# Kernel tuning notes

Measured on AMD Instinct MI355X. Metric: run time of the kernel, lower is better.

## Reference

```python
import jax, jax.numpy as jnp
import numpy as np

B, S, D = 8, 2048, 64
H = 128


def setup_inputs() -> dict:
    key = jax.random.key(0)
    k = jax.random.split(key, 5)
    X = jax.random.normal(k[0], (B, S, D), dtype=jnp.float32)
    Wi = jax.random.normal(k[1], (H, D), dtype=jnp.float32)          # init_layer weight, std=1
    bi = jax.random.normal(k[2], (H,), dtype=jnp.float32)            # init_layer bias, std=1
    Wa = jax.random.normal(k[3], (H * H, D + 1), dtype=jnp.float32) / jnp.sqrt(H)  # vf_A, std=1/sqrt(H)
    Wb = jax.random.normal(k[4], (H, D + 1), dtype=jnp.float32)      # vf_B, std=1
    return {"X": X, "Wi": Wi, "bi": bi, "Wa": Wa, "Wb": Wb}


def reference(X, Wi, bi, Wa, Wb):
    b, s, d = X.shape
    dt = 1.0 / (s - 1)
    # inp: time channel (constant dt) concatenated with scaled input -> [b, s, d+1]
    inp = jnp.concatenate([jnp.full((b, s, 1), dt, dtype=X.dtype), X * dt], axis=-1)
    y0 = X[:, 0] @ Wi.T + bi                       # [b, H]
    Bs = jnp.einsum('bsk,hk->bsh', inp[:, 1:], Wb)  # [b, s-1, H]

    def step(y, xs):
        inp_t, b_t = xs                            # [b, d+1], [b, H]
        A = (inp_t @ Wa.T).reshape(b, H, H)        # per-step transition matrix
        y_new = y + jnp.einsum('bij,bj->bi', A, y) + b_t
        return y_new, y_new

    xs = (jnp.swapaxes(inp[:, 1:], 0, 1), jnp.swapaxes(Bs, 0, 1))  # time-major
    _, ys_rest = jax.lax.scan(step, y0, xs)        # [s-1, b, H]
    ys = jnp.concatenate([y0[:, None, :], jnp.swapaxes(ys_rest, 0, 1)], axis=1)
    return ys
```

## Files before the change

### kernel.cpp

```cpp
#include <hip/hip_runtime.h>
#include <hip/hip_fp16.h>


typedef _Float16 h8 __attribute__((ext_vector_type(8)));
typedef float v4f __attribute__((ext_vector_type(4)));
typedef unsigned int uint;

constexpr int B_ = 8, S_ = 2048, D_ = 64, H_ = 128;
constexpr int T_ = S_ - 1;
constexpr int KD = D_ + 1;
constexpr float DTC = 1.0f / 2047.0f;
constexpr int L_ = 8;
constexpr int LSH = 3;
constexpr int NC = 256;

__global__ __launch_bounds__(256) void k_prep0(const float* __restrict__ Wa,
                                               _Float16* __restrict__ Wa16B,
                                               float* __restrict__ Wa0,
                                               const float* __restrict__ X,
                                               _Float16* __restrict__ Xs16) {
  int bx = blockIdx.x;
  if (bx < 4096) {
    int idx = bx * 256 + threadIdx.x;
    int r = idx >> 6, kk = idx & 63;
    int rt = r >> 4, n = r & 15;
    int kb = kk >> 5, q = (kk >> 3) & 3, jj = kk & 7;
    float v = Wa[(size_t)r * KD + 1 + kk];
    Wa16B[((((size_t)rt * 2 + kb) * 4 + q) * 16 + n) * 8 + jj] = (_Float16)v;
    if (kk == 0) Wa0[r] = Wa[(size_t)r * KD];
  } else {
    int idx = (bx - 4096) * 256 + threadIdx.x;
    if (idx < B_ * T_ * 64) {
      int bt = idx >> 6, d = idx & 63;
      int b = bt / T_, s = bt - b * T_;
      Xs16[(size_t)bt * 64 + d] = (_Float16)(X[((size_t)b * S_ + s + 1) * D_ + d] * DTC);
    }
  }
}

__global__ __launch_bounds__(256) void k_prep1(const float* __restrict__ X,
                                               const float* __restrict__ Wb,
                                               float* __restrict__ Bs,
                                               const float* __restrict__ Wi,
                                               const float* __restrict__ bi,
                                               float* __restrict__ out,
                                               float* __restrict__ yb) {
  int tid = threadIdx.x;
  if (blockIdx.x >= 1024) {
    int b = blockIdx.x - 1024;
    __shared__ float xs0[D_];
    if (tid < D_) xs0[tid] = X[(size_t)b * S_ * D_ + tid];
    __syncthreads();
    if (tid < H_) {
      float acc = bi[tid];
      const float* wr = Wi + tid * D_;
#pragma unroll 8
      for (int d = 0; d < D_; d++) acc += xs0[d] * wr[d];
      out[(size_t)b * S_ * H_ + tid] = acc;
      yb[(size_t)(b * NC + 0) * H_ + tid] = acc;
    }
    return;
  }
  __shared__ float wb_s[H_ * KD];
  __shared__ float xs[16][D_ + 4];
  int bt0 = blockIdx.x * 16;
  for (int i = tid; i < H_ * KD; i += 256) wb_s[i] = Wb[i];
  for (int i = tid; i < 16 * D_; i += 256) {
    int sl = i >> 6, d = i & 63;
    int btg = bt0 + sl;
    float v = 0.f;
    if (btg < B_ * T_) {
      int b = btg / T_, s = btg - b * T_;
      v = X[((size_t)b * S_ + s + 1) * D_ + d] * DTC;
    }
    xs[sl][d] = v;
  }
  __syncthreads();
  int h = tid & 127, sh = tid >> 7;
  const float* wrow = &wb_s[h * KD];
  for (int u = 0; u < 8; u++) {
    int sl = sh * 8 + u;
    int btg = bt0 + sl;
    if (btg >= B_ * T_) break;
    float acc = wrow[0] * DTC;
#pragma unroll 8
    for (int d = 0; d < D_; d++) acc += xs[sl][d] * wrow[1 + d];
    Bs[(size_t)btg * H_ + h] = acc;
  }
}

__global__ __launch_bounds__(256) void k_amat(const _Float16* __restrict__ Xs16,
                                              const _Float16* __restrict__ Wa16B,
                                              const float* __restrict__ Wa0,
                                              _Float16* __restrict__ A_sl,
                                              int c0, int scShift) {
  __shared__ _Float16 sb[32 * 528];
  int tid = threadIdx.x;
  int w = tid >> 6, lane = tid & 63;
  int n = lane & 15, q = lane >> 4;
  int rowbase = blockIdx.x * 32;
  int SCm = ((1 << scShift) << LSH) - 1;

  h8 af[2][2];
#pragma unroll
  for (int mi = 0; mi < 2; mi++) {
    int sidx = rowbase + mi * 16 + n;
    int b = sidx >> (scShift + LSH);
    int rem = sidx & SCm;
    int cc = rem >> LSH, l = rem & (L_ - 1);
    int s = (c0 + cc) * L_ + l;
    if (s >= T_) s = T_ - 1;
    size_t btg = (size_t)b * T_ + s;
#pragma unroll
    for (int kb = 0; kb < 2; kb++)
      af[mi][kb] = *(const h8*)(Xs16 + btg * 64 + kb * 32 + q * 8);
  }

  v4f acc[2][8];
#pragma unroll
  for (int nj = 0; nj < 8; nj++) {
    int ct_g = blockIdx.y * 32 + w * 8 + nj;
    float binit = DTC * Wa0[ct_g * 16 + n];
    h8 bf0 = *(const h8*)(Wa16B + ((((size_t)ct_g * 2 + 0) * 4 + q) * 16 + n) * 8);
    h8 bf1 = *(const h8*)(Wa16B + ((((size_t)ct_g * 2 + 1) * 4 + q) * 16 + n) * 8);
#pragma unroll
    for (int mi = 0; mi < 2; mi++) {
      v4f a;
      a[0] = binit; a[1] = binit; a[2] = binit; a[3] = binit;
      a = __builtin_amdgcn_mfma_f32_16x16x32_f16(af[mi][0], bf0, a, 0, 0, 0);
      a = __builtin_amdgcn_mfma_f32_16x16x32_f16(af[mi][1], bf1, a, 0, 0, 0);
      acc[mi][nj] = a;
    }
  }
#pragma unroll
  for (int mi = 0; mi < 2; mi++)
#pragma unroll
    for (int nj = 0; nj < 8; nj++)
#pragma unroll
      for (int reg = 0; reg < 4; reg++)
        sb[(mi * 16 + q * 4 + reg) * 528 + w * 128 + ((nj * 16 + n) ^ (q * 16))] =
            (_Float16)acc[mi][nj][reg];
  __syncthreads();
#pragma unroll
  for (int it = 0; it < 8; it++) {
    int idx = tid + it * 256;
    int t = idx >> 6, u4 = idx & 63;
    int qt = (t >> 2) & 3;
    uint4 val = *(const uint4*)&sb[t * 528 + ((u4 * 8) ^ (qt * 16))];
    *(uint4*)(A_sl + (size_t)(rowbase + t) * 16384 + blockIdx.y * 512 + u4 * 8) = val;
  }
}

__global__ __launch_bounds__(256) void k_chunkmap(const _Float16* __restrict__ A_sl,
                                                  const float* __restrict__ Bs,
                                                  _Float16* __restrict__ Mr,
                                                  float* __restrict__ vch,
                                                  int c0, int scShift) {
  __shared__ _Float16 Dt[128 * 136];
  __shared__ float v32[128];
  int tid = threadIdx.x;
  int w = tid >> 6, lane = tid & 63;
  int n = lane & 15, q = lane >> 4;
  int chunk = blockIdx.x;
  int SC = 1 << scShift;
  int b = chunk >> scShift;
  int cc = chunk & (SC - 1);
  int c = c0 + cc;
  int sbase = c * L_;
  int nsteps = min(L_, T_ - sbase);
  const _Float16* Abase = A_sl + (size_t)chunk * L_ * 16384;
  size_t btb = (size_t)b * T_ + sbase;

#pragma unroll
  for (int it = 0; it < 8; it++) {
    int idx = tid + it * 256;
    int rowl = idx & 127, c8 = (idx >> 7) * 8;
    uint4 pk = *(const uint4*)(Abase + rowl * 128 + c8);
    const _Float16* hp = (const _Float16*)&pk;
#pragma unroll
    for (int cx = 0; cx < 8; cx++) Dt[(c8 + cx) * 136 + rowl] = hp[cx];
  }
  if (tid < 128) v32[tid] = Bs[btb * 128 + tid];
  h8 idE, idO;
#pragma unroll
  for (int jj = 0; jj < 8; jj++) {
    idE[jj] = (_Float16)((q * 8 + jj == n) ? 1.f : 0.f);
    idO[jj] = (_Float16)((q * 8 + jj == 16 + n) ? 1.f : 0.f);
  }
  __syncthreads();

  v4f acc[2][8];
#pragma unroll
  for (int mi = 0; mi < 2; mi++) {
    int row0 = (2 * w + mi) * 16 + q * 4;
#pragma unroll
    for (int nj = 0; nj < 8; nj++) {
      int col = nj * 16 + n;
      union { uint2 u; _Float16 h[4]; } m2;
      m2.u = *(const uint2*)&Dt[col * 136 + row0];
#pragma unroll
      for (int reg = 0; reg < 4; reg++) acc[mi][nj][reg] = (float)m2.h[reg];
    }
  }

  int r0 = 2 * w * 16 + n, r1 = r0 + 16;
  h8 afA[2][4], afB[2][4];

#define LOADA(dst, l)                                                                \
  {                                                                                  \
    const _Float16* Ag = Abase + (size_t)(l) * 16384;                                \
    _Pragma("unroll")                                                                \
    for (int mi = 0; mi < 2; mi++)                                                   \
      _Pragma("unroll")                                                              \
      for (int kb = 0; kb < 4; kb++)                                                 \
        dst[mi][kb] = *(const h8*)(Ag + ((2 * w + mi) * 16 + n) * 128 + kb * 32 + q * 8); \
  }

#define STEPQ(af, l)                                                                 \
  {                                                                                  \
    _Pragma("unroll")                                                                \
    for (int nj = 0; nj < 8; nj++) {                                                 \
      h8 bfr[4];                                                                     \
      _Pragma("unroll")                                                              \
      for (int kb = 0; kb < 4; kb++)                                                 \
        bfr[kb] = *(const h8*)&Dt[(nj * 16 + n) * 136 + kb * 32 + q * 8];            \
      _Pragma("unroll")                                                              \
      for (int mi = 0; mi < 2; mi++) {                                               \
        _Pragma("unroll")                                                            \
        for (int kb = 0; kb < 4; kb++)                                               \
          acc[mi][nj] = __builtin_amdgcn_mfma_f32_16x16x32_f16(af[mi][kb], bfr[kb], acc[mi][nj], 0, 0, 0); \
        acc[mi][nj] = __builtin_amdgcn_mfma_f32_16x16x32_f16(                        \
            af[mi][nj >> 1], (nj & 1) ? idO : idE, acc[mi][nj], 0, 0, 0);            \
      }                                                                              \
    }                                                                                \
    float dv0 = 0.f, dv1 = 0.f;                                                      \
    _Pragma("unroll")                                                                \
    for (int kb = 0; kb < 4; kb++) {                                                 \
      float4 p0 = *(const float4*)&v32[kb * 32 + q * 8];                             \
      float4 p1 = *(const float4*)&v32[kb * 32 + q * 8 + 4];                         \
      float vk[8] = {p0.x, p0.y, p0.z, p0.w, p1.x, p1.y, p1.z, p1.w};                \
      _Pragma("unroll")                                                              \
      for (int jj = 0; jj < 8; jj++) {                                               \
        dv0 += (float)af[0][kb][jj] * vk[jj];                                        \
        dv1 += (float)af[1][kb][jj] * vk[jj];                                        \
      }                                                                              \
    }                                                                                \
    dv0 += __shfl_xor(dv0, 16); dv0 += __shfl_xor(dv0, 32);                          \
    dv1 += __shfl_xor(dv1, 16); dv1 += __shfl_xor(dv1, 32);                          \
    float vold0 = v32[r0], vold1 = v32[r1];                                          \
    float bs0 = 0.f, bs1 = 0.f;                                                      \
    if (q == 0) {                                                                    \
      bs0 = Bs[(btb + (l)) * 128 + r0];                                              \
      bs1 = Bs[(btb + (l)) * 128 + r1];                                              \
    }                                                                                \
    __syncthreads();                                                                 \
    _Pragma("unroll")                                                                \
    for (int mi = 0; mi < 2; mi++) {                                                 \
      int row0 = (2 * w + mi) * 16 + q * 4;                                          \
      _Pragma("unroll")                                                              \
      for (int nj = 0; nj < 8; nj++) {                                               \
        int col = nj * 16 + n;                                                       \
        union { _Float16 h[4]; uint2 u; } pk;                                        \
        _Pragma("unroll")                                                            \
        for (int reg = 0; reg < 4; reg++) pk.h[reg] = (_Float16)acc[mi][nj][reg];    \
        *(uint2*)&Dt[col * 136 + row0] = pk.u;                                       \
      }                                                                              \
    }                                                                                \
    if (q == 0) {                                                                    \
      v32[r0] = vold0 + dv0 + bs0;                                                   \
      v32[r1] = vold1 + dv1 + bs1;                                                   \
    }                                                                                \
    __syncthreads();                                                                 \
  }

  LOADA(afA, 1);
  for (int l = 1; l < nsteps; l += 2) {
    if (l + 1 < nsteps) LOADA(afB, l + 1);
    STEPQ(afA, l);
    if (l + 2 < nsteps) LOADA(afA, l + 2);
    if (l + 1 < nsteps) STEPQ(afB, l + 1);
  }
#undef LOADA
#undef STEPQ

#pragma unroll
  for (int mi = 0; mi < 2; mi++) {
    int row0 = (2 * w + mi) * 16 + q * 4;
#pragma unroll
    for (int nj = 0; nj < 8; nj++) {
      int col = nj * 16 + n;
#pragma unroll
      for (int reg = 0; reg < 4; reg++)
        Dt[(row0 + reg) * 136 + col] = (_Float16)acc[mi][nj][reg];
    }
  }
  __syncthreads();
  _Float16* og = Mr + (size_t)chunk * 16384;
#pragma unroll
  for (int it = 0; it < 8; it++) {
    int idx = tid + it * 256;
    int rowl = idx >> 4, ch = idx & 15;
    uint4 val = *(const uint4*)&Dt[rowl * 136 + ch * 8];
    *(uint4*)(og + rowl * 128 + ch * 8) = val;
  }
  if (tid < 128) vch[(size_t)chunk * 128 + tid] = v32[tid];
}

__global__ __launch_bounds__(256) void k_comp4(const _Float16* __restrict__ in_map,
                                               const float* __restrict__ in_v,
                                               _Float16* __restrict__ out_map,
                                               float* __restrict__ out_v) {
  __shared__ _Float16 Dt[128 * 136];
  __shared__ float v32[128];
  int tid = threadIdx.x;
  int w = tid >> 6, lane = tid & 63;
  int n = lane & 15, q = lane >> 4;
  size_t nbase = (size_t)blockIdx.x * 4;

  const _Float16* P0 = in_map + nbase * 16384;
#pragma unroll
  for (int it = 0; it < 8; it++) {
    int idx = tid + it * 256;
    int rowl = idx & 127, c8 = (idx >> 7) * 8;
    uint4 pk = *(const uint4*)(P0 + rowl * 128 + c8);
    const _Float16* hp = (const _Float16*)&pk;
#pragma unroll
    for (int cx = 0; cx < 8; cx++) Dt[(c8 + cx) * 136 + rowl] = hp[cx];
  }
  if (tid < 128) v32[tid] = in_v[nbase * 128 + tid];
  h8 idE, idO;
#pragma unroll
  for (int jj = 0; jj < 8; jj++) {
    idE[jj] = (_Float16)((q * 8 + jj == n) ? 1.f : 0.f);
    idO[jj] = (_Float16)((q * 8 + jj == 16 + n) ? 1.f : 0.f);
  }
  __syncthreads();

  v4f acc[2][8];
#pragma unroll
  for (int mi = 0; mi < 2; mi++) {
    int row0 = (2 * w + mi) * 16 + q * 4;
#pragma unroll
    for (int nj = 0; nj < 8; nj++) {
      int col = nj * 16 + n;
      union { uint2 u; _Float16 h[4]; } m2;
      m2.u = *(const uint2*)&Dt[col * 136 + row0];
#pragma unroll
      for (int reg = 0; reg < 4; reg++) acc[mi][nj][reg] = (float)m2.h[reg];
    }
  }

  int r0 = 2 * w * 16 + n, r1 = r0 + 16;
  for (int j = 1; j < 4; j++) {
    const _Float16* Pj = in_map + (nbase + j) * 16384;
    h8 af[2][4];
#pragma unroll
    for (int mi = 0; mi < 2; mi++)
#pragma unroll
      for (int kb = 0; kb < 4; kb++)
        af[mi][kb] = *(const h8*)(Pj + ((2 * w + mi) * 16 + n) * 128 + kb * 32 + q * 8);
#pragma unroll
    for (int nj = 0; nj < 8; nj++) {
      h8 bfr[4];
#pragma unroll
      for (int kb = 0; kb < 4; kb++)
        bfr[kb] = *(const h8*)&Dt[(nj * 16 + n) * 136 + kb * 32 + q * 8];
#pragma unroll
      for (int mi = 0; mi < 2; mi++) {
#pragma unroll
        for (int kb = 0; kb < 4; kb++)
          acc[mi][nj] = __builtin_amdgcn_mfma_f32_16x16x32_f16(af[mi][kb], bfr[kb], acc[mi][nj], 0, 0, 0);
        acc[mi][nj] = __builtin_amdgcn_mfma_f32_16x16x32_f16(
            af[mi][nj >> 1], (nj & 1) ? idO : idE, acc[mi][nj], 0, 0, 0);
      }
    }
    float dv0 = 0.f, dv1 = 0.f;
#pragma unroll
    for (int kb = 0; kb < 4; kb++) {
      float4 p0 = *(const float4*)&v32[kb * 32 + q * 8];
      float4 p1 = *(const float4*)&v32[kb * 32 + q * 8 + 4];
      float vk[8] = {p0.x, p0.y, p0.z, p0.w, p1.x, p1.y, p1.z, p1.w};
#pragma unroll
      for (int jj = 0; jj < 8; jj++) {
        dv0 += (float)af[0][kb][jj] * vk[jj];
        dv1 += (float)af[1][kb][jj] * vk[jj];
      }
    }
    dv0 += __shfl_xor(dv0, 16); dv0 += __shfl_xor(dv0, 32);
    dv1 += __shfl_xor(dv1, 16); dv1 += __shfl_xor(dv1, 32);
    float vold0 = v32[r0], vold1 = v32[r1];
    float vj0 = 0.f, vj1 = 0.f;
    if (q == 0) {
      vj0 = in_v[(nbase + j) * 128 + r0];
      vj1 = in_v[(nbase + j) * 128 + r1];
    }
    __syncthreads();
#pragma unroll
    for (int mi = 0; mi < 2; mi++) {
      int row0 = (2 * w + mi) * 16 + q * 4;
#pragma unroll
      for (int nj = 0; nj < 8; nj++) {
        int col = nj * 16 + n;
        union { _Float16 h[4]; uint2 u; } pk;
#pragma unroll
        for (int reg = 0; reg < 4; reg++) pk.h[reg] = (_Float16)acc[mi][nj][reg];
        *(uint2*)&Dt[col * 136 + row0] = pk.u;
      }
    }
    if (q == 0) {
      v32[r0] = vold0 + dv0 + vj0;
      v32[r1] = vold1 + dv1 + vj1;
    }
    __syncthreads();
  }
#pragma unroll
  for (int mi = 0; mi < 2; mi++) {
    int row0 = (2 * w + mi) * 16 + q * 4;
#pragma unroll
    for (int nj = 0; nj < 8; nj++) {
      int col = nj * 16 + n;
#pragma unroll
      for (int reg = 0; reg < 4; reg++)
        Dt[(row0 + reg) * 136 + col] = (_Float16)acc[mi][nj][reg];
    }
  }
  __syncthreads();
  _Float16* og = out_map + (size_t)blockIdx.x * 16384;
#pragma unroll
  for (int it = 0; it < 8; it++) {
    int idx = tid + it * 256;
    int rowl = idx >> 4, ch = idx & 15;
    uint4 val = *(const uint4*)&Dt[rowl * 136 + ch * 8];
    *(uint4*)(og + rowl * 128 + ch * 8) = val;
  }
  if (tid < 128) out_v[(size_t)blockIdx.x * 128 + tid] = v32[tid];
}

__global__ __launch_bounds__(256) void k_chainsuper(const _Float16* __restrict__ Sr,
                                                    const float* __restrict__ sv,
                                                    float* __restrict__ yb,
                                                    int c0, int scShift) {
  int b = blockIdx.x, tid = threadIdx.x;
  int NS = 1 << (scShift - 2);
  int i = tid >> 1, hh = tid & 1;
  __shared__ float ybuf[128];
  __shared__ float red[128];
  if (tid < 128) ybuf[tid] = yb[(size_t)(b * NC + c0) * 128 + tid];
  __syncthreads();

  uint4 arA[8], arB[8];
  float svA, svB;

#define LOADS(ar, svv, s)                                                            \
  {                                                                                  \
    const uint4* p = (const uint4*)(Sr + (size_t)(b * NS + (s)) * 16384 + i * 128 + hh * 64); \
    _Pragma("unroll")                                                                \
    for (int u = 0; u < 8; u++) ar[u] = p[u];                                        \
    svv = sv[(size_t)(b * NS + (s)) * 128 + i];                                      \
  }

#define STEPS(ar, svv, s)                                                            \
  {                                                                                  \
    float pt = 0.f;                                                                  \
    _Pragma("unroll")                                                                \
    for (int u = 0; u < 8; u++) {                                                    \
      union { uint4 v; _Float16 h[8]; } wv; wv.v = ar[u];                            \
      _Pragma("unroll")                                                              \
      for (int k = 0; k < 8; k++) pt += (float)wv.h[k] * ybuf[hh * 64 + u * 8 + k];  \
    }                                                                                \
    if (hh) red[i] = pt;                                                             \
    __syncthreads();                                                                 \
    if (!hh) {                                                                       \
      float yn = ybuf[i] + pt + red[i] + svv;                                        \
      int cg = c0 + 4 * ((s) + 1);                                                   \
      if (cg < NC) yb[(size_t)(b * NC + cg) * 128 + i] = yn;                         \
      ybuf[i] = yn;                                                                  \
    }                                                                                \
    __syncthreads();                                                                 \
  }

  LOADS(arA, svA, 0);
  int s = 0;
  for (; s + 1 < NS; s += 2) {
    LOADS(arB, svB, s + 1);
    STEPS(arA, svA, s);
    if (s + 2 < NS) LOADS(arA, svA, s + 2);
    STEPS(arB, svB, s + 1);
  }
  if (s < NS) STEPS(arA, svA, s);
#undef LOADS
#undef STEPS
}

__global__ __launch_bounds__(256) void k_emit(const _Float16* __restrict__ A_sl,
                                              const float* __restrict__ Bs,
                                              const _Float16* __restrict__ Mr,
                                              const float* __restrict__ vch,
                                              const float* __restrict__ yb,
                                              float* __restrict__ out,
                                              int c0, int scShift) {
  int tid = threadIdx.x;
  int SC = 1 << scShift;
  int b = blockIdx.x >> scShift;
  int cc = blockIdx.x & (SC - 1);
  int c = c0 + cc;
  int i = tid >> 1, hh = tid & 1;
  __shared__ float ybuf[128];
  __shared__ float red[128];
  int kpre = cc & 3;
  int cbase = c - kpre;
  if (tid < 128) ybuf[tid] = yb[(size_t)(b * NC + cbase) * 128 + tid];
  __syncthreads();
  size_t node0 = ((size_t)b << scShift) + (cc & ~3);

  uint4 arA[8], arB[8];
  float bsA, bsB;

  for (int j = 0; j < kpre; j++) {
    const uint4* p = (const uint4*)(Mr + (node0 + j) * 16384 + i * 128 + hh * 64);
#pragma unroll
    for (int u = 0; u < 8; u++) arA[u] = p[u];
    float vv = vch[(node0 + j) * 128 + i];
    float pt = 0.f;
#pragma unroll
    for (int u = 0; u < 8; u++) {
      union { uint4 v; _Float16 h[8]; } wv; wv.v = arA[u];
#pragma unroll
      for (int k = 0; k < 8; k++) pt += (float)wv.h[k] * ybuf[hh * 64 + u * 8 + k];
    }
    if (hh) red[i] = pt;
    __syncthreads();
    if (!hh) {
      float yn = ybuf[i] + pt + red[i] + vv;
      ybuf[i] = yn;
    }
    __syncthreads();
  }

  int nst = min(L_, T_ - c * L_);
  size_t sidx0 = (size_t)blockIdx.x * L_;
  size_t btb = (size_t)b * T_ + c * L_;

#define LOADR(ar, bsv, l)                                                            \
  {                                                                                  \
    const uint4* p = (const uint4*)(A_sl + (sidx0 + (l)) * 16384 + i * 128 + hh * 64); \
    _Pragma("unroll")                                                                \
    for (int u = 0; u < 8; u++) ar[u] = p[u];                                        \
    bsv = Bs[(btb + (l)) * 128 + i];                                                 \
  }

#define STEPE(ar, bsv, l)                                                            \
  {                                                                                  \
    float pt = 0.f;                                                                  \
    _Pragma("unroll")                                                                \
    for (int u = 0; u < 8; u++) {                                                    \
      union { uint4 v; _Float16 h[8]; } wv; wv.v = ar[u];                            \
      _Pragma("unroll")                                                              \
      for (int k = 0; k < 8; k++) pt += (float)wv.h[k] * ybuf[hh * 64 + u * 8 + k];  \
    }                                                                                \
    if (hh) red[i] = pt;                                                             \
    __syncthreads();                                                                 \
    if (!hh) {                                                                       \
      float yn = ybuf[i] + pt + red[i] + bsv;                                        \
      out[((size_t)b * S_ + (size_t)(c * L_ + (l) + 1)) * 128 + i] = yn;             \
      ybuf[i] = yn;                                                                  \
    }                                                                                \
    __syncthreads();                                                                 \
  }

  LOADR(arA, bsA, 0);
  for (int l = 0; l < nst; l += 2) {
    if (l + 1 < nst) LOADR(arB, bsB, l + 1);
    STEPE(arA, bsA, l);
    if (l + 2 < nst) LOADR(arA, bsA, l + 2);
    if (l + 1 < nst) STEPE(arB, bsB, l + 1);
  }
#undef LOADR
#undef STEPE
}

__global__ __launch_bounds__(256) void k_seq(const float* __restrict__ X,
                                             const float* __restrict__ Wa,
                                             const float* __restrict__ Wb,
                                             float* __restrict__ out) {
  int b = blockIdx.x, tid = threadIdx.x;
  int i = tid >> 1, hh = tid & 1;
  __shared__ float y[H_], red[H_], xs[D_], bts[H_];
  if (tid < H_) y[tid] = out[(size_t)b * S_ * H_ + tid];
  __syncthreads();
  for (int t = 1; t < S_; t++) {
    if (tid < D_) xs[tid] = X[((size_t)b * S_ + t) * D_ + tid] * DTC;
    __syncthreads();
    if (tid < H_) {
      const float* wr = Wb + tid * KD;
      float acc = wr[0] * DTC;
#pragma unroll 8
      for (int d = 0; d < D_; d++) acc += xs[d] * wr[1 + d];
      bts[tid] = acc;
    }
    float part = 0.f;
    const float* yhalf = &y[hh * 64];
    for (int j = 0; j < 64; j++) {
      const float* wr = Wa + ((size_t)(i * H_) + hh * 64 + j) * KD;
      float a = wr[0] * DTC;
#pragma unroll 8
      for (int d = 0; d < D_; d++) a += xs[d] * wr[1 + d];
      part += a * yhalf[j];
    }
    if (hh) red[i] = part;
    __syncthreads();
    if (!hh) {
      float yn = y[i] + part + red[i] + bts[i];
      out[((size_t)b * S_ + t) * H_ + i] = yn;
      y[i] = yn;
    }
    __syncthreads();
  }
}

__global__ __launch_bounds__(128) void k_y0f(const float* __restrict__ X,
                                             const float* __restrict__ Wi,
                                             const float* __restrict__ bi,
                                             float* __restrict__ out) {
  int b = blockIdx.x, h = threadIdx.x;
  __shared__ float xs[D_];
  if (h < D_) xs[h] = X[(size_t)b * S_ * D_ + h];
  __syncthreads();
  float acc = bi[h];
  const float* wr = Wi + h * D_;
#pragma unroll 8
  for (int d = 0; d < D_; d++) acc += xs[d] * wr[d];
  out[(size_t)b * S_ * H_ + h] = acc;
}

extern "C" void kernel_launch(void* const* d_in, const int* in_sizes, int n_in,
                              void* d_out, int out_size, void* d_ws, size_t ws_size,
                              hipStream_t stream) {
  (void)in_sizes; (void)n_in; (void)out_size;
  const float* X  = (const float*)d_in[0];
  const float* Wi = (const float*)d_in[1];
  const float* bi = (const float*)d_in[2];
  const float* Wa = (const float*)d_in[3];
  const float* Wb = (const float*)d_in[4];
  float* out = (float*)d_out;
  char* ws = (char*)d_ws;

  size_t off = 0;
  auto alloc = [&](size_t bytes) { size_t o = off; off = (off + bytes + 255) & ~(size_t)255; return o; };
  size_t oBs  = alloc((size_t)B_ * T_ * 128 * 4);
  size_t oYb  = alloc((size_t)B_ * NC * 128 * 4);
  size_t oWaB = alloc((size_t)64 * 16384 * 2);
  size_t oWa0 = alloc((size_t)16384 * 4);
  size_t oXs  = alloc((size_t)B_ * T_ * 64 * 2);
  size_t fixed = off;

  const size_t APC  = (size_t)B_ * L_ * 16384 * 2;
  const size_t MRPC = (size_t)B_ * 16384 * 2;
  const size_t VCPC = (size_t)B_ * 128 * 4;
  const size_t SRPC = (size_t)B_ * 16384 * 2 / 4;
  const size_t SVPC = (size_t)B_ * 128;
  const size_t PER_SC = APC + MRPC + VCPC + SRPC + SVPC + 5 * 256;

  int SC = 0;
  if (ws_size > fixed) {
    size_t avail = ws_size - fixed;
    SC = 64;
    while (SC >= 4 && (size_t)SC * PER_SC > avail) SC >>= 1;
    if (SC < 4) SC = 0;
  }
  if (SC < 4) {
    k_y0f<<<B_, 128, 0, stream>>>(X, Wi, bi, out);
    k_seq<<<B_, 256, 0, stream>>>(X, Wa, Wb, out);
    return;
  }
  int scShift = __builtin_ctz(SC);

  size_t oMr = alloc((size_t)SC * MRPC);
  size_t oVc = alloc((size_t)SC * VCPC);
  size_t oSr = alloc((size_t)SC * SRPC);
  size_t oSv = alloc((size_t)SC * SVPC);
  size_t oA  = alloc((size_t)SC * APC);

  float*    Bs    = (float*)(ws + oBs);
  float*    yb    = (float*)(ws + oYb);
  _Float16* Wa16B = (_Float16*)(ws + oWaB);
  float*    Wa0   = (float*)(ws + oWa0);
  _Float16* Xs16  = (_Float16*)(ws + oXs);
  _Float16* Mr    = (_Float16*)(ws + oMr);
  float*    vch   = (float*)(ws + oVc);
  _Float16* Sr    = (_Float16*)(ws + oSr);
  float*    sv    = (float*)(ws + oSv);
  _Float16* A_sl  = (_Float16*)(ws + oA);

  k_prep0<<<4096 + 4094, 256, 0, stream>>>(Wa, Wa16B, Wa0, X, Xs16);
  k_prep1<<<1024 + B_, 256, 0, stream>>>(X, Wb, Bs, Wi, bi, out, yb);

  int nslices = NC / SC;
  int chunks = B_ * SC;
  int amat_gx = (B_ * SC * L_) / 32;
  for (int si = 0; si < nslices; si++) {
    int c0 = si * SC;
    k_amat<<<dim3(amat_gx, 32), 256, 0, stream>>>(Xs16, Wa16B, Wa0, A_sl, c0, scShift);
    k_chunkmap<<<chunks, 256, 0, stream>>>(A_sl, Bs, Mr, vch, c0, scShift);
    k_comp4<<<chunks / 4, 256, 0, stream>>>(Mr, vch, Sr, sv);
    k_chainsuper<<<B_, 256, 0, stream>>>(Sr, sv, yb, c0, scShift);
    k_emit<<<chunks, 256, 0, stream>>>(A_sl, Bs, Mr, vch, yb, out, c0, scShift);
  }
}
```

Before: 608.5 us.

## Fuse per-slice scan stages into one cooperative kernel with grid syncs

```diff
diff --git a/kernel.cpp b/kernel.cpp
--- a/kernel.cpp
+++ b/kernel.cpp
@@ -1,5 +1,8 @@
 #include <hip/hip_runtime.h>
 #include <hip/hip_fp16.h>
+#include <hip/hip_cooperative_groups.h>
+
+namespace cg = cooperative_groups;
 
 
 typedef _Float16 h8 __attribute__((ext_vector_type(8)));
@@ -14,78 +17,72 @@
 constexpr int LSH = 3;
 constexpr int NC = 256;
 
-__global__ __launch_bounds__(256) void k_prep0(const float* __restrict__ Wa,
-                                               _Float16* __restrict__ Wa16B,
-                                               float* __restrict__ Wa0,
-                                               const float* __restrict__ X,
-                                               _Float16* __restrict__ Xs16) {
-  int bx = blockIdx.x;
+__global__ __launch_bounds__(256) void k_prep(const float* __restrict__ Wa,
+                                              _Float16* __restrict__ Wa16B,
+                                              float* __restrict__ Wa0,
+                                              const float* __restrict__ X,
+                                              _Float16* __restrict__ Xs16,
+                                              const float* __restrict__ Wb,
+                                              float* __restrict__ Bs,
+                                              const float* __restrict__ Wi,
+                                              const float* __restrict__ bi,
+                                              float* __restrict__ out,
+                                              float* __restrict__ yb) {
+  __shared__ float wb_s[H_ * KD];
+  __shared__ float xs[16][D_ + 4];
+  int bx = blockIdx.x, tid = threadIdx.x;
   if (bx < 4096) {
-    int idx = bx * 256 + threadIdx.x;
+    int idx = bx * 256 + tid;
     int r = idx >> 6, kk = idx & 63;
     int rt = r >> 4, n = r & 15;
     int kb = kk >> 5, q = (kk >> 3) & 3, jj = kk & 7;
     float v = Wa[(size_t)r * KD + 1 + kk];
     Wa16B[((((size_t)rt * 2 + kb) * 4 + q) * 16 + n) * 8 + jj] = (_Float16)v;
     if (kk == 0) Wa0[r] = Wa[(size_t)r * KD];
-  } else {
-    int idx = (bx - 4096) * 256 + threadIdx.x;
+  } else if (bx < 8190) {
+    int idx = (bx - 4096) * 256 + tid;
     if (idx < B_ * T_ * 64) {
       int bt = idx >> 6, d = idx & 63;
       int b = bt / T_, s = bt - b * T_;
       Xs16[(size_t)bt * 64 + d] = (_Float16)(X[((size_t)b * S_ + s + 1) * D_ + d] * DTC);
     }
-  }
-}
-
-__global__ __launch_bounds__(256) void k_prep1(const float* __restrict__ X,
-                                               const float* __restrict__ Wb,
-                                               float* __restrict__ Bs,
-                                               const float* __restrict__ Wi,
-                                               const float* __restrict__ bi,
-                                               float* __restrict__ out,
-                                               float* __restrict__ yb) {
-  int tid = threadIdx.x;
-  if (blockIdx.x >= 1024) {
-    int b = blockIdx.x - 1024;
-    __shared__ float xs0[D_];
-    if (tid < D_) xs0[tid] = X[(size_t)b * S_ * D_ + tid];
+  } else if (bx < 9214) {
+    int bt0 = (bx - 8190) * 16;
+    for (int i2 = tid; i2 < H_ * KD; i2 += 256) wb_s[i2] = Wb[i2];
+    for (int i2 = tid; i2 < 16 * D_; i2 += 256) {
+      int sl = i2 >> 6, d = i2 & 63;
+      int btg = bt0 + sl;
+      float v = 0.f;
+      if (btg < B_ * T_) {
+        int b = btg / T_, s = btg - b * T_;
+        v = X[((size_t)b * S_ + s + 1) * D_ + d] * DTC;
+      }
+      xs[sl][d] = v;
+    }
+    __syncthreads();
+    int h = tid & 127, sh = tid >> 7;
+    const float* wrow = &wb_s[h * KD];
+    for (int u = 0; u < 8; u++) {
+      int sl = sh * 8 + u;
+      int btg = bt0 + sl;
+      if (btg >= B_ * T_) break;
+      float acc = wrow[0] * DTC;
+#pragma unroll 8
+      for (int d = 0; d < D_; d++) acc += xs[sl][d] * wrow[1 + d];
+      Bs[(size_t)btg * H_ + h] = acc;
+    }
+  } else {
+    int b = bx - 9214;
+    if (tid < D_) xs[0][tid] = X[(size_t)b * S_ * D_ + tid];
     __syncthreads();
     if (tid < H_) {
       float acc = bi[tid];
       const float* wr = Wi + tid * D_;
 #pragma unroll 8
-      for (int d = 0; d < D_; d++) acc += xs0[d] * wr[d];
+      for (int d = 0; d < D_; d++) acc += xs[0][d] * wr[d];
       out[(size_t)b * S_ * H_ + tid] = acc;
       yb[(size_t)(b * NC + 0) * H_ + tid] = acc;
     }
-    return;
-  }
-  __shared__ float wb_s[H_ * KD];
-  __shared__ float xs[16][D_ + 4];
-  int bt0 = blockIdx.x * 16;
-  for (int i = tid; i < H_ * KD; i += 256) wb_s[i] = Wb[i];
-  for (int i = tid; i < 16 * D_; i += 256) {
-    int sl = i >> 6, d = i & 63;
-    int btg = bt0 + sl;
-    float v = 0.f;
-    if (btg < B_ * T_) {
-      int b = btg / T_, s = btg - b * T_;
-      v = X[((size_t)b * S_ + s + 1) * D_ + d] * DTC;
-    }
-    xs[sl][d] = v;
-  }
-  __syncthreads();
-  int h = tid & 127, sh = tid >> 7;
-  const float* wrow = &wb_s[h * KD];
-  for (int u = 0; u < 8; u++) {
-    int sl = sh * 8 + u;
-    int btg = bt0 + sl;
-    if (btg >= B_ * T_) break;
-    float acc = wrow[0] * DTC;
-#pragma unroll 8
-    for (int d = 0; d < D_; d++) acc += xs[sl][d] * wrow[1 + d];
-    Bs[(size_t)btg * H_ + h] = acc;
   }
 }
 
@@ -151,17 +148,14 @@
   }
 }
 
-__global__ __launch_bounds__(256) void k_chunkmap(const _Float16* __restrict__ A_sl,
-                                                  const float* __restrict__ Bs,
-                                                  _Float16* __restrict__ Mr,
-                                                  float* __restrict__ vch,
-                                                  int c0, int scShift) {
-  __shared__ _Float16 Dt[128 * 136];
-  __shared__ float v32[128];
-  int tid = threadIdx.x;
+__device__ __forceinline__ void chunkmap_body(const _Float16* __restrict__ A_sl,
+                                              const float* __restrict__ Bs,
+                                              _Float16* __restrict__ Mr,
+                                              float* __restrict__ vch,
+                                              int c0, int scShift, int chunk, int tid,
+                                              _Float16* Dt, float* v32) {
   int w = tid >> 6, lane = tid & 63;
   int n = lane & 15, q = lane >> 4;
-  int chunk = blockIdx.x;
   int SC = 1 << scShift;
   int b = chunk >> scShift;
   int cc = chunk & (SC - 1);
@@ -306,16 +300,15 @@
   if (tid < 128) vch[(size_t)chunk * 128 + tid] = v32[tid];
 }
 
-__global__ __launch_bounds__(256) void k_comp4(const _Float16* __restrict__ in_map,
-                                               const float* __restrict__ in_v,
-                                               _Float16* __restrict__ out_map,
-                                               float* __restrict__ out_v) {
-  __shared__ _Float16 Dt[128 * 136];
-  __shared__ float v32[128];
-  int tid = threadIdx.x;
+__device__ __forceinline__ void comp4_body(const _Float16* __restrict__ in_map,
+                                           const float* __restrict__ in_v,
+                                           _Float16* __restrict__ out_map,
+                                           float* __restrict__ out_v,
+                                           int outIdx, int tid,
+                                           _Float16* Dt, float* v32) {
   int w = tid >> 6, lane = tid & 63;
   int n = lane & 15, q = lane >> 4;
-  size_t nbase = (size_t)blockIdx.x * 4;
+  size_t nbase = (size_t)outIdx * 4;
 
   const _Float16* P0 = in_map + nbase * 16384;
 #pragma unroll
@@ -425,7 +418,7 @@
     }
   }
   __syncthreads();
-  _Float16* og = out_map + (size_t)blockIdx.x * 16384;
+  _Float16* og = out_map + (size_t)outIdx * 16384;
 #pragma unroll
   for (int it = 0; it < 8; it++) {
     int idx = tid + it * 256;
@@ -433,18 +426,16 @@
     uint4 val = *(const uint4*)&Dt[rowl * 136 + ch * 8];
     *(uint4*)(og + rowl * 128 + ch * 8) = val;
   }
-  if (tid < 128) out_v[(size_t)blockIdx.x * 128 + tid] = v32[tid];
-}
-
-__global__ __launch_bounds__(256) void k_chainsuper(const _Float16* __restrict__ Sr,
-                                                    const float* __restrict__ sv,
-                                                    float* __restrict__ yb,
-                                                    int c0, int scShift) {
-  int b = blockIdx.x, tid = threadIdx.x;
+  if (tid < 128) out_v[(size_t)outIdx * 128 + tid] = v32[tid];
+}
+
+__device__ __forceinline__ void chainsuper_body(const _Float16* __restrict__ Sr,
+                                                const float* __restrict__ sv,
+                                                float* __restrict__ yb,
+                                                int c0, int scShift, int b, int tid,
+                                                float* ybuf, float* red) {
   int NS = 1 << (scShift - 2);
   int i = tid >> 1, hh = tid & 1;
-  __shared__ float ybuf[128];
-  __shared__ float red[128];
   if (tid < 128) ybuf[tid] = yb[(size_t)(b * NC + c0) * 128 + tid];
   __syncthreads();
 
@@ -492,39 +483,37 @@
 #undef STEPS
 }
 
-__global__ __launch_bounds__(256) void k_emit(const _Float16* __restrict__ A_sl,
-                                              const float* __restrict__ Bs,
-                                              const _Float16* __restrict__ Mr,
-                                              const float* __restrict__ vch,
-                                              const float* __restrict__ yb,
-                                              float* __restrict__ out,
-                                              int c0, int scShift) {
-  int tid = threadIdx.x;
-  int SC = 1 << scShift;
-  int b = blockIdx.x >> scShift;
-  int cc = blockIdx.x & (SC - 1);
-  int c = c0 + cc;
+__device__ __forceinline__ void emit_body(const _Float16* __restrict__ A_sl,
+                                          const float* __restrict__ Bs,
+                                          const _Float16* __restrict__ Mr,
+                                          const float* __restrict__ vch,
+                                          const float* __restrict__ yb,
+                                          float* __restrict__ out,
+                                          int tid, int b, int c, int kpre, int cbase,
+                                          int nst, size_t node0, size_t sidx0, size_t btb,
+                                          uint4* arA, float bsA, uint4* arP, float vvP,
+                                          float* ybuf, float* red) {
   int i = tid >> 1, hh = tid & 1;
-  __shared__ float ybuf[128];
-  __shared__ float red[128];
-  int kpre = cc & 3;
-  int cbase = c - kpre;
   if (tid < 128) ybuf[tid] = yb[(size_t)(b * NC + cbase) * 128 + tid];
   __syncthreads();
-  size_t node0 = ((size_t)b << scShift) + (cc & ~3);
-
-  uint4 arA[8], arB[8];
-  float bsA, bsB;
 
   for (int j = 0; j < kpre; j++) {
-    const uint4* p = (const uint4*)(Mr + (node0 + j) * 16384 + i * 128 + hh * 64);
-#pragma unroll
-    for (int u = 0; u < 8; u++) arA[u] = p[u];
-    float vv = vch[(node0 + j) * 128 + i];
+    uint4 ar[8];
+    float vv;
+    if (j == 0) {
+#pragma unroll
+      for (int u = 0; u < 8; u++) ar[u] = arP[u];
+      vv = vvP;
+    } else {
+      const uint4* p = (const uint4*)(Mr + (node0 + j) * 16384 + i * 128 + hh * 64);
+#pragma unroll
+      for (int u = 0; u < 8; u++) ar[u] = p[u];
+      vv = vch[(node0 + j) * 128 + i];
+    }
     float pt = 0.f;
 #pragma unroll
     for (int u = 0; u < 8; u++) {
-      union { uint4 v; _Float16 h[8]; } wv; wv.v = arA[u];
+      union { uint4 v; _Float16 h[8]; } wv; wv.v = ar[u];
 #pragma unroll
       for (int k = 0; k < 8; k++) pt += (float)wv.h[k] * ybuf[hh * 64 + u * 8 + k];
     }
@@ -537,9 +526,8 @@
     __syncthreads();
   }
 
-  int nst = min(L_, T_ - c * L_);
-  size_t sidx0 = (size_t)blockIdx.x * L_;
-  size_t btb = (size_t)b * T_ + c * L_;
+  uint4 arB[8];
+  float bsB;
 
 #define LOADR(ar, bsv, l)                                                            \
   {                                                                                  \
@@ -568,7 +556,6 @@
     __syncthreads();                                                                 \
   }
 
-  LOADR(arA, bsA, 0);
   for (int l = 0; l < nst; l += 2) {
     if (l + 1 < nst) LOADR(arB, bsB, l + 1);
     STEPE(arA, bsA, l);
@@ -577,6 +564,130 @@
   }
 #undef LOADR
 #undef STEPE
+}
+
+__global__ __launch_bounds__(256) void k_chunkmap(const _Float16* __restrict__ A_sl,
+                                                  const float* __restrict__ Bs,
+                                                  _Float16* __restrict__ Mr,
+                                                  float* __restrict__ vch,
+                                                  int c0, int scShift) {
+  __shared__ _Float16 Dt[128 * 136];
+  __shared__ float v32[128];
+  chunkmap_body(A_sl, Bs, Mr, vch, c0, scShift, blockIdx.x, threadIdx.x, Dt, v32);
+}
+
+__global__ __launch_bounds__(256) void k_comp4(const _Float16* __restrict__ in_map,
+                                               const float* __restrict__ in_v,
+                                               _Float16* __restrict__ out_map,
+                                               float* __restrict__ out_v) {
+  __shared__ _Float16 Dt[128 * 136];
+  __shared__ float v32[128];
+  comp4_body(in_map, in_v, out_map, out_v, blockIdx.x, threadIdx.x, Dt, v32);
+}
+
+__global__ __launch_bounds__(256) void k_chainsuper(const _Float16* __restrict__ Sr,
+                                                    const float* __restrict__ sv,
+                                                    float* __restrict__ yb,
+                                                    int c0, int scShift) {
+  __shared__ float ybuf[128];
+  __shared__ float red[128];
+  chainsuper_body(Sr, sv, yb, c0, scShift, blockIdx.x, threadIdx.x, ybuf, red);
+}
+
+__global__ __launch_bounds__(256) void k_emit(const _Float16* __restrict__ A_sl,
+                                              const float* __restrict__ Bs,
+                                              const _Float16* __restrict__ Mr,
+                                              const float* __restrict__ vch,
+                                              const float* __restrict__ yb,
+                                              float* __restrict__ out,
+                                              int c0, int scShift) {
+  __shared__ float ybuf[128];
+  __shared__ float red[128];
+  int tid = threadIdx.x;
+  int SC = 1 << scShift;
+  int b = blockIdx.x >> scShift;
+  int cc = blockIdx.x & (SC - 1);
+  int c = c0 + cc;
+  int i = tid >> 1, hh = tid & 1;
+  int kpre = cc & 3;
+  int cbase = c - kpre;
+  size_t node0 = ((size_t)b << scShift) + (cc & ~3);
+  int nst = min(L_, T_ - c * L_);
+  size_t sidx0 = (size_t)blockIdx.x * L_;
+  size_t btb = (size_t)b * T_ + c * L_;
+  uint4 arA[8], arP[8];
+  float bsA, vvP = 0.f;
+  {
+    const uint4* p = (const uint4*)(A_sl + sidx0 * 16384 + i * 128 + hh * 64);
+#pragma unroll
+    for (int u = 0; u < 8; u++) arA[u] = p[u];
+    bsA = Bs[btb * 128 + i];
+  }
+  if (kpre > 0) {
+    const uint4* p2 = (const uint4*)(Mr + node0 * 16384 + i * 128 + hh * 64);
+#pragma unroll
+    for (int u = 0; u < 8; u++) arP[u] = p2[u];
+    vvP = vch[node0 * 128 + i];
+  }
+  emit_body(A_sl, Bs, Mr, vch, yb, out, tid, b, c, kpre, cbase, nst, node0, sidx0, btb,
+            arA, bsA, arP, vvP, ybuf, red);
+}
+
+__global__ __launch_bounds__(256, 2) void k_slice(const _Float16* __restrict__ A_sl,
+                                                  const float* __restrict__ Bs,
+                                                  _Float16* __restrict__ Mr,
+                                                  float* __restrict__ vch,
+                                                  _Float16* __restrict__ Sr,
+                                                  float* __restrict__ sv,
+                                                  float* __restrict__ yb,
+                                                  float* __restrict__ out,
+                                                  int c0, int scShift) {
+  __shared__ _Float16 Dt[128 * 136];
+  __shared__ float v32[128];
+  __shared__ float ybuf[128];
+  __shared__ float red[128];
+  int tid = threadIdx.x;
+  cg::grid_group grid = cg::this_grid();
+
+  chunkmap_body(A_sl, Bs, Mr, vch, c0, scShift, blockIdx.x, tid, Dt, v32);
+  grid.sync();
+
+  if (blockIdx.x < (int)(gridDim.x >> 2))
+    comp4_body(Mr, vch, Sr, sv, blockIdx.x, tid, Dt, v32);
+  grid.sync();
+
+  int SC = 1 << scShift;
+  int eb = blockIdx.x >> scShift;
+  int ecc = blockIdx.x & (SC - 1);
+  int ec = c0 + ecc;
+  int i = tid >> 1, hh = tid & 1;
+  int kpre = ecc & 3;
+  int cbase = ec - kpre;
+  size_t node0 = ((size_t)eb << scShift) + (ecc & ~3);
+  int nst = min(L_, T_ - ec * L_);
+  size_t sidx0 = (size_t)blockIdx.x * L_;
+  size_t btb = (size_t)eb * T_ + ec * L_;
+  uint4 arA[8], arP[8];
+  float bsA, vvP = 0.f;
+  {
+    const uint4* p = (const uint4*)(A_sl + sidx0 * 16384 + i * 128 + hh * 64);
+#pragma unroll
+    for (int u = 0; u < 8; u++) arA[u] = p[u];
+    bsA = Bs[btb * 128 + i];
+  }
+  if (kpre > 0) {
+    const uint4* p2 = (const uint4*)(Mr + node0 * 16384 + i * 128 + hh * 64);
+#pragma unroll
+    for (int u = 0; u < 8; u++) arP[u] = p2[u];
+    vvP = vch[node0 * 128 + i];
+  }
+
+  if (blockIdx.x < B_)
+    chainsuper_body(Sr, sv, yb, c0, scShift, blockIdx.x, tid, ybuf, red);
+  grid.sync();
+
+  emit_body(A_sl, Bs, Mr, vch, yb, out, tid, eb, ec, kpre, cbase, nst, node0, sidx0, btb,
+            arA, bsA, arP, vvP, ybuf, red);
 }
 
 __global__ __launch_bounds__(256) void k_seq(const float* __restrict__ X,
@@ -692,18 +803,41 @@
   float*    sv    = (float*)(ws + oSv);
   _Float16* A_sl  = (_Float16*)(ws + oA);
 
-  k_prep0<<<4096 + 4094, 256, 0, stream>>>(Wa, Wa16B, Wa0, X, Xs16);
-  k_prep1<<<1024 + B_, 256, 0, stream>>>(X, Wb, Bs, Wi, bi, out, yb);
+  k_prep<<<9222, 256, 0, stream>>>(Wa, Wa16B, Wa0, X, Xs16, Wb, Bs, Wi, bi, out, yb);
+
+  static int coopNB = -1;
+  if (coopNB < 0) {
+    int nb = 0;
+    coopNB = (hipOccupancyMaxActiveBlocksPerMultiprocessor(&nb, k_slice, 256, 0) == hipSuccess)
+                 ? nb : 0;
+  }
 
   int nslices = NC / SC;
   int chunks = B_ * SC;
   int amat_gx = (B_ * SC * L_) / 32;
+  bool useCoop = ((size_t)coopNB * 256 >= (size_t)chunks);
   for (int si = 0; si < nslices; si++) {
     int c0 = si * SC;
     k_amat<<<dim3(amat_gx, 32), 256, 0, stream>>>(Xs16, Wa16B, Wa0, A_sl, c0, scShift);
-    k_chunkmap<<<chunks, 256, 0, stream>>>(A_sl, Bs, Mr, vch, c0, scShift);
-    k_comp4<<<chunks / 4, 256, 0, stream>>>(Mr, vch, Sr, sv);
-    k_chainsuper<<<B_, 256, 0, stream>>>(Sr, sv, yb, c0, scShift);
-    k_emit<<<chunks, 256, 0, stream>>>(A_sl, Bs, Mr, vch, yb, out, c0, scShift);
-  }
-}
+    bool done = false;
+    if (useCoop) {
+      const _Float16* aA = A_sl; const float* aB = Bs;
+      _Float16* aM = Mr; float* aV = vch;
+      _Float16* aS = Sr; float* aSv = sv;
+      float* aY = yb; float* aO = out;
+      int ac0 = c0, asc = scShift;
+      void* args[] = {&aA, &aB, &aM, &aV, &aS, &aSv, &aY, &aO, &ac0, &asc};
+      if (hipLaunchCooperativeKernel((const void*)k_slice, dim3(chunks), dim3(256),
+                                     args, 0, stream) == hipSuccess)
+        done = true;
+      else
+        useCoop = false;
+    }
+    if (!done) {
+      k_chunkmap<<<chunks, 256, 0, stream>>>(A_sl, Bs, Mr, vch, c0, scShift);
+      k_comp4<<<chunks / 4, 256, 0, stream>>>(Mr, vch, Sr, sv);
+      k_chainsuper<<<B_, 256, 0, stream>>>(Sr, sv, yb, c0, scShift);
+      k_emit<<<chunks, 256, 0, stream>>>(A_sl, Bs, Mr, vch, yb, out, c0, scShift);
+    }
+  }
+}
```

Result: slower. 671.4 us (+10.3%).
